# Kernel optimization log

Hardware: AMD Instinct MI355X
Metric: run time of the kernel (lower is better)

The kernel has to match this reference:

```python
import jax, jax.numpy as jnp
import numpy as np

N = 50000          # nodes
E = 800000         # directed edges (before self loops)
H = 2              # attention heads
NEG_SLOPE = 0.2    # PyG GATv2 default
EPS = 1e-5         # GraphNorm eps
DIMS = [(3, 64), (64, 64), (64, 64)]


def _gatv2_layer(x, Wl, Wr, att, b, src, dst):
    # x: [N, din]; Wl, Wr: [din, H*C]; att: [H, C]; b: [C]
    n = x.shape[0]
    h, c = att.shape
    xl = (x @ Wl).reshape(n, h, c)   # source-side transform
    xr = (x @ Wr).reshape(n, h, c)   # target-side transform
    # edge-wise GATv2 score: a . leaky_relu(xl[j] + xr[i])
    e = jax.nn.leaky_relu(xl[src] + xr[dst], NEG_SLOPE)      # [E, H, C]
    logit = jnp.einsum('ehc,hc->eh', e, att)                 # [E, H]
    # segment softmax over incoming edges of each target node
    m = jax.ops.segment_max(logit, dst, num_segments=n)      # [N, H]
    a = jnp.exp(logit - m[dst])
    z = jax.ops.segment_sum(a, dst, num_segments=n)
    alpha = a / z[dst]                                       # [E, H]
    out = jax.ops.segment_sum(alpha[:, :, None] * xl[src], dst, num_segments=n)  # [N, H, C]
    return out.mean(axis=1) + b                              # concat=False -> head mean


def _graph_norm(x, w, b, ms):
    # single-graph GraphNorm: x -> w * (x - ms*mean) / sqrt(var + eps) + b
    mu = x.mean(axis=0)
    o = x - ms * mu
    var = (o * o).mean(axis=0)
    return w * o * jax.lax.rsqrt(var + EPS) + b


def setup_inputs() -> dict:
    key = jax.random.key(0)
    ks = jax.random.split(key, 2 + 3 * len(DIMS))
    inp = {
        'x': jax.random.normal(ks[0], (N, 3), dtype=jnp.float32),
        'edge_index': jax.random.randint(ks[1], (2, E), 0, N, dtype=jnp.int32),
    }
    for i, (din, dout) in enumerate(DIMS, start=1):
        k0, k1, k2 = ks[2 + 3 * (i - 1):2 + 3 * i]
        s_in = np.float32(1.0 / np.sqrt(din))
        s_att = np.float32(1.0 / np.sqrt(dout))
        inp[f'Wl{i}'] = jax.random.normal(k0, (din, H * dout), dtype=jnp.float32) * s_in
        inp[f'Wr{i}'] = jax.random.normal(k1, (din, H * dout), dtype=jnp.float32) * s_in
        inp[f'att{i}'] = jax.random.normal(k2, (H, dout), dtype=jnp.float32) * s_att
        inp[f'b{i}'] = jnp.zeros((dout,), dtype=jnp.float32)
        inp[f'gw{i}'] = jnp.ones((dout,), dtype=jnp.float32)
        inp[f'gb{i}'] = jnp.zeros((dout,), dtype=jnp.float32)
        inp[f'gm{i}'] = jnp.ones((dout,), dtype=jnp.float32)
    return inp


def reference(x, edge_index,
              Wl1, Wr1, att1, b1, gw1, gb1, gm1,
              Wl2, Wr2, att2, b2, gw2, gb2, gm2,
              Wl3, Wr3, att3, b3, gw3, gb3, gm3):
    n = x.shape[0]
    loop = jnp.arange(n, dtype=edge_index.dtype)
    src = jnp.concatenate([edge_index[0], loop])  # add_self_loops=True
    dst = jnp.concatenate([edge_index[1], loop])
    layers = [(Wl1, Wr1, att1, b1, gw1, gb1, gm1),
              (Wl2, Wr2, att2, b2, gw2, gb2, gm2),
              (Wl3, Wr3, att3, b3, gw3, gb3, gm3)]
    for Wl, Wr, att, b, gw, gb, gm in layers:
        x = _gatv2_layer(x, Wl, Wr, att, b, src, dst)
        x = jax.nn.relu(_graph_norm(x, gw, gb, gm))
    return x
```

## Files before the change

kernel.cpp:

```cpp
#include <hip/hip_runtime.h>
#include <math.h>

#define NN 50000
#define NE 800000
#define TE (NE + NN)
#define HC 128
#define NEG_SLOPE 0.2f
#define EPSV 1e-5f
#define NBUCK 64
#define GGRID 782
#define WTB 128
#define ZB 52
#define ZERO_N4 18644

typedef __attribute__((ext_vector_type(8))) short bf16x8;
typedef __attribute__((ext_vector_type(4))) float f32x4;
union BfU { uint4 u; bf16x8 b; };

__device__ __forceinline__ unsigned short f2bf(float x) {
    unsigned u = __float_as_uint(x);
    unsigned r = (u + 0x7fff + ((u >> 16) & 1)) >> 16;
    return (unsigned short)r;
}


__global__ __launch_bounds__(256) void count_k(const int* __restrict__ dst,
                                               int* __restrict__ cnt,
                                               int* __restrict__ rank) {
    int e = blockIdx.x * 256 + threadIdx.x;
    if (e >= TE) return;
    int d = (e < NE) ? dst[e] : (e - NE);
    rank[e] = atomicAdd(&cnt[d], 1);
}

__global__ __launch_bounds__(1024) void scan1_k(const int* __restrict__ cnt,
                                                int* __restrict__ excl,
                                                int* __restrict__ aux) {
    __shared__ int wsum[16];
    int tid = threadIdx.x;
    int gid = blockIdx.x * 1024 + tid;
    int lane = tid & 63, wid = tid >> 6;
    int v = (gid < NN) ? cnt[gid] : 0;
    int x = v;
#pragma unroll
    for (int off = 1; off < 64; off <<= 1) {
        int t = __shfl_up(x, off, 64);
        if (lane >= off) x += t;
    }
    if (lane == 63) wsum[wid] = x;
    __syncthreads();
    if (wid == 0 && lane < 16) {
        int y = wsum[lane];
#pragma unroll
        for (int off = 1; off < 16; off <<= 1) {
            int t = __shfl_up(y, off, 64);
            if (lane >= off) y += t;
        }
        wsum[lane] = y;
    }
    __syncthreads();
    int base = (wid > 0) ? wsum[wid - 1] : 0;
    int incl = base + x;
    if (gid < NN) excl[gid] = incl - v;
    if (tid == 1023) aux[blockIdx.x] = incl;
}

__global__ __launch_bounds__(256) void scatter_k(const int* __restrict__ srcp,
                                                 const int* __restrict__ dstp,
                                                 const int* __restrict__ excl,
                                                 const int* __restrict__ aux,
                                                 const int* __restrict__ rank,
                                                 int* __restrict__ row_ptr,
                                                 int* __restrict__ col,
                                                 int nblk) {
    __shared__ int auxs[64];
    if (threadIdx.x < 64) {
        int lane = threadIdx.x;
        int v = (lane < nblk) ? aux[lane] : 0;
        int x = v;
#pragma unroll
        for (int off = 1; off < 64; off <<= 1) {
            int t = __shfl_up(x, off, 64);
            if (lane >= off) x += t;
        }
        auxs[lane] = x - v;
    }
    __syncthreads();
    int e = blockIdx.x * 256 + threadIdx.x;
    if (e >= TE) return;
    if (e <= NN) row_ptr[e] = (e == NN) ? TE : excl[e] + auxs[e >> 10];
    int s, d;
    if (e < NE) { s = srcp[e]; d = dstp[e]; } else { s = e - NE; d = s; }
    col[excl[d] + auxs[d >> 10] + rank[e]] = s << 8;
}

__device__ __forceinline__ void store_xlp(char* xlp, int row, int c0, const float* a) {
    unsigned hsel = (unsigned)c0 >> 6;
    unsigned dd = (unsigned)c0 & 31;
    unsigned sub = (c0 & 32) ? 2u : 0u;
    char* q = xlp + (size_t)row * 256 + hsel * 128 + 4 * dd + sub;
#pragma unroll
    for (int j = 0; j < 4; ++j)
        *(unsigned short*)(q + 4 * j) = f2bf(a[j]);
}


__global__ __launch_bounds__(256) void init_k(const float* __restrict__ x,
                                              const float* __restrict__ Wl1,
                                              const float* __restrict__ Wr1,
                                              char* __restrict__ xlp,
                                              float* __restrict__ xr,
                                              const float* __restrict__ Wl2,
                                              const float* __restrict__ Wr2,
                                              const float* __restrict__ Wl3,
                                              const float* __restrict__ Wr3,
                                              unsigned short* __restrict__ wt2,
                                              unsigned short* __restrict__ wt3,
                                              float4* __restrict__ zero4) {
    __shared__ float xs[32][72];
    __shared__ float ws[32][260];
    int b = blockIdx.x;
    int tid = threadIdx.x;

    if (b >= GGRID) {
        if (b < GGRID + WTB) {
            int idx = (b - GGRID) * 256 + tid;
            int l = idx >> 14;
            int rem = idx & 16383;
            int k = rem >> 8;
            int c = rem & 255;
            const float* W = (l == 0) ? (c < 128 ? Wl2 : Wr2) : (c < 128 ? Wl3 : Wr3);
            float v = W[k * 128 + (c & 127)];
            unsigned short* wt = (l == 0) ? wt2 : wt3;
            wt[c * 64 + k] = f2bf(v);
        } else {
            float4 zv; zv.x = zv.y = zv.z = zv.w = 0.f;
            for (int i = (b - GGRID - WTB) * 256 + tid; i < ZERO_N4; i += ZB * 256)
                zero4[i] = zv;
        }
        return;
    }

    int row0 = b * 64;
    int row_t = (tid >> 5) * 8;
    int c0 = (tid & 31) * 4;
    const int K = 3;

    float acc0[8][4];
    float acc1[8][4];
#pragma unroll
    for (int i = 0; i < 8; ++i)
#pragma unroll
        for (int j = 0; j < 4; ++j) { acc0[i][j] = 0.f; acc1[i][j] = 0.f; }

    for (int i = tid; i < 64 * K; i += 256) {
        int r = i / K;
        int k = i - r * K;
        int row = row0 + r;
        xs[k][r] = (row < NN) ? x[(size_t)row * K + k] : 0.f;
    }
    for (int i = tid; i < K * 64; i += 256) {
        int k = i >> 6;
        int cq = i & 63;
        const float* srcp = (cq < 32) ? &Wl1[(size_t)k * 128 + cq * 4]
                                      : &Wr1[(size_t)k * 128 + (cq - 32) * 4];
        float4 v = *(const float4*)srcp;
        *(float4*)&ws[k][cq * 4] = v;
    }
    __syncthreads();
    for (int k = 0; k < K; ++k) {
        float4 a0 = *(float4*)&xs[k][row_t];
        float4 a1 = *(float4*)&xs[k][row_t + 4];
        float4 b0 = *(float4*)&ws[k][c0];
        float4 b1 = *(float4*)&ws[k][c0 + 128];
        float av[8] = {a0.x, a0.y, a0.z, a0.w, a1.x, a1.y, a1.z, a1.w};
        float bl[4] = {b0.x, b0.y, b0.z, b0.w};
        float br[4] = {b1.x, b1.y, b1.z, b1.w};
#pragma unroll
        for (int i = 0; i < 8; ++i)
#pragma unroll
            for (int j = 0; j < 4; ++j) {
                acc0[i][j] += av[i] * bl[j];
                acc1[i][j] += av[i] * br[j];
            }
    }
#pragma unroll
    for (int i = 0; i < 8; ++i) {
        int row = row0 + row_t + i;
        if (row < NN) {
            store_xlp(xlp, row, c0, acc0[i]);
            float4 o1; o1.x = acc1[i][0]; o1.y = acc1[i][1]; o1.z = acc1[i][2]; o1.w = acc1[i][3];
            *(float4*)&xr[(size_t)row * HC + c0] = o1;
        }
    }
}

__device__ __forceinline__ void reduce_stats(const float* __restrict__ stats,
                                             const float* __restrict__ gw,
                                             const float* __restrict__ gb,
                                             const float* __restrict__ gm,
                                             float (*part)[128],
                                             float* __restrict__ cf_out) {
    int tid = threadIdx.x;
    int w = tid >> 6;
    int lane = tid & 63;
    float s = 0.f, s2 = 0.f;
    for (int b = 16 * w; b < 16 * w + 16; ++b) {
        s += stats[b * 128 + lane];
        s2 += stats[b * 128 + 64 + lane];
    }
    part[w][lane] = s;
    part[w][64 + lane] = s2;
    __syncthreads();
    if (tid < 64) {
        int c = tid;
        float sum = (part[0][c] + part[1][c]) + (part[2][c] + part[3][c]);
        float sum2 = (part[0][64 + c] + part[1][64 + c]) + (part[2][64 + c] + part[3][64 + c]);
        float inv_n = 1.f / (float)NN;
        float mu = sum * inv_n;
        float ex2 = sum2 * inv_n;
        float g = gm[c];
        float var = ex2 - 2.f * g * mu * mu + g * g * mu * mu;
        float rs = rsqrtf(var + EPSV);
        cf_out[c] = gw[c] * rs;
        cf_out[64 + c] = gb[c] - gw[c] * rs * g * mu;
    }
    __syncthreads();
}


__global__ __launch_bounds__(256) void gemm_mfma(const unsigned* __restrict__ hbf,
                                                 const float* __restrict__ stats,
                                                 const float* __restrict__ gw,
                                                 const float* __restrict__ gb,
                                                 const float* __restrict__ gm,
                                                 const unsigned short* __restrict__ wt,
                                                 char* __restrict__ xlp,
                                                 float* __restrict__ xr,
                                                 int n) {
    __shared__ unsigned short xs[64][72];
    __shared__ float part[4][128];
    __shared__ float cfS[128];
    int tid = threadIdx.x;
    int row0 = blockIdx.x * 64;

    reduce_stats(stats, gw, gb, gm, part, cfS);

    {
        int r = tid >> 2;
        int q = tid & 3;
        int row = row0 + r;
        unsigned pk[8];
        if (row < n) {
            const unsigned* hp = hbf + (size_t)row * 32 + (q & 1) * 16;
            uint4 u0 = *(const uint4*)(hp + 0);
            uint4 u1 = *(const uint4*)(hp + 4);
            uint4 u2 = *(const uint4*)(hp + 8);
            uint4 u3 = *(const uint4*)(hp + 12);
            unsigned hv[16] = {u0.x, u0.y, u0.z, u0.w, u1.x, u1.y, u1.z, u1.w,
                               u2.x, u2.y, u2.z, u2.w, u3.x, u3.y, u3.z, u3.w};
            bool hi = (q >> 1) != 0;
#pragma unroll
            for (int i = 0; i < 4; ++i) {
                float4 v;
                v.x = hi ? __uint_as_float(hv[4 * i + 0] & 0xffff0000u) : __uint_as_float(hv[4 * i + 0] << 16);
                v.y = hi ? __uint_as_float(hv[4 * i + 1] & 0xffff0000u) : __uint_as_float(hv[4 * i + 1] << 16);
                v.z = hi ? __uint_as_float(hv[4 * i + 2] & 0xffff0000u) : __uint_as_float(hv[4 * i + 2] << 16);
                v.w = hi ? __uint_as_float(hv[4 * i + 3] & 0xffff0000u) : __uint_as_float(hv[4 * i + 3] << 16);
                float4 cw = *(const float4*)&cfS[q * 16 + 4 * i];
                float4 cb = *(const float4*)&cfS[64 + q * 16 + 4 * i];
                float r0 = fmaxf(fmaf(cw.x, v.x, cb.x), 0.f);
                float r1 = fmaxf(fmaf(cw.y, v.y, cb.y), 0.f);
                float r2 = fmaxf(fmaf(cw.z, v.z, cb.z), 0.f);
                float r3 = fmaxf(fmaf(cw.w, v.w, cb.w), 0.f);
                pk[2 * i]     = (unsigned)f2bf(r0) | ((unsigned)f2bf(r1) << 16);
                pk[2 * i + 1] = (unsigned)f2bf(r2) | ((unsigned)f2bf(r3) << 16);
            }
        } else {
#pragma unroll
            for (int i = 0; i < 8; ++i) pk[i] = 0;
        }
        uint4* dst = (uint4*)&xs[r][q * 16];
        dst[0] = make_uint4(pk[0], pk[1], pk[2], pk[3]);
        dst[1] = make_uint4(pk[4], pk[5], pk[6], pk[7]);
    }
    __syncthreads();

    int w = tid >> 6;
    int lane = tid & 63;
    int m = lane & 15;
    int quad = lane >> 4;

    BfU a0, a1;
    a0.u = *(const uint4*)&xs[16 * w + m][quad * 8];
    a1.u = *(const uint4*)&xs[16 * w + m][32 + quad * 8];

    const char* wtb = (const char*)wt + (size_t)(m * 128 + quad * 16);

    f32x4 acc[16];
#pragma unroll
    for (int c = 0; c < 16; ++c) acc[c] = (f32x4){0.f, 0.f, 0.f, 0.f};
#pragma unroll
    for (int c = 0; c < 16; ++c) {
        BfU b0, b1;
        b0.u = *(const uint4*)(wtb + c * 2048);
        b1.u = *(const uint4*)(wtb + c * 2048 + 64);
        acc[c] = __builtin_amdgcn_mfma_f32_16x16x32_bf16(a0.b, b0.b, acc[c], 0, 0, 0);
        acc[c] = __builtin_amdgcn_mfma_f32_16x16x32_bf16(a1.b, b1.b, acc[c], 0, 0, 0);
    }

    int rbase = row0 + 16 * w + quad * 4;
#pragma unroll
    for (int c = 8; c < 16; ++c) {
        int colx = 16 * (c - 8) + m;
#pragma unroll
        for (int r = 0; r < 4; ++r) {
            int row = rbase + r;
            if (row < n) xr[(size_t)row * 128 + colx] = acc[c][r];
        }
    }
#pragma unroll
    for (int pi = 0; pi < 4; ++pi) {
        int c = (pi & 1) + (pi >> 1) * 4;
        int head = pi >> 1;
        int dd = (pi & 1) * 16 + m;
#pragma unroll
        for (int r = 0; r < 4; ++r) {
            int row = rbase + r;
            if (row < n) {
                unsigned val = (unsigned)f2bf(acc[c][r]) | ((unsigned)f2bf(acc[c + 2][r]) << 16);
                *(unsigned*)(xlp + (size_t)row * 256 + head * 128 + 4 * dd) = val;
            }
        }
    }
}


__device__ __forceinline__ void unpack8(uint4 q, float* l) {
    l[0] = __uint_as_float(q.x << 16);
    l[1] = __uint_as_float(q.x & 0xffff0000u);
    l[2] = __uint_as_float(q.y << 16);
    l[3] = __uint_as_float(q.y & 0xffff0000u);
    l[4] = __uint_as_float(q.z << 16);
    l[5] = __uint_as_float(q.z & 0xffff0000u);
    l[6] = __uint_as_float(q.w << 16);
    l[7] = __uint_as_float(q.w & 0xffff0000u);
}

__device__ __forceinline__ float logit_part(const float* l,
                                            float4 xv0, float4 xv1,
                                            float4 a0, float4 a1) {
    float u1 = 0.f, u2 = 0.f, t;
    t = l[0] + xv0.x; u1 = fmaf(a0.x, t, u1); u2 = fmaf(a0.x, fabsf(t), u2);
    t = l[1] + xv1.x; u1 = fmaf(a1.x, t, u1); u2 = fmaf(a1.x, fabsf(t), u2);
    t = l[2] + xv0.y; u1 = fmaf(a0.y, t, u1); u2 = fmaf(a0.y, fabsf(t), u2);
    t = l[3] + xv1.y; u1 = fmaf(a1.y, t, u1); u2 = fmaf(a1.y, fabsf(t), u2);
    t = l[4] + xv0.z; u1 = fmaf(a0.z, t, u1); u2 = fmaf(a0.z, fabsf(t), u2);
    t = l[5] + xv1.z; u1 = fmaf(a1.z, t, u1); u2 = fmaf(a1.z, fabsf(t), u2);
    t = l[6] + xv0.w; u1 = fmaf(a0.w, t, u1); u2 = fmaf(a0.w, fabsf(t), u2);
    t = l[7] + xv1.w; u1 = fmaf(a1.w, t, u1); u2 = fmaf(a1.w, fabsf(t), u2);
    return fmaf(0.6f, u1, 0.4f * u2);
}

__device__ __forceinline__ float head_reduce(float x) {
    x += __int_as_float(__builtin_amdgcn_mov_dpp(__float_as_int(x), 0xB1, 0xF, 0xF, true));
    x += __int_as_float(__builtin_amdgcn_mov_dpp(__float_as_int(x), 0x4E, 0xF, 0xF, true));
    x += __shfl_xor(x, 4, 64);
    return x;
}

__device__ __forceinline__ void attn_pair(const char* __restrict__ xlp, int lp16,
                                          int off0, int off1, bool v0, bool v1,
                                          float4 xv0, float4 xv1,
                                          float4 a0, float4 a1,
                                          float* o, float& zacc) {
    uint4 q0 = *(const uint4*)(xlp + (unsigned)(off0 + lp16));
    uint4 q1 = *(const uint4*)(xlp + (unsigned)(off1 + lp16));
    float l0[8], l1[8];
    unpack8(q0, l0);
    unpack8(q1, l1);
    float w0 = head_reduce(logit_part(l0, xv0, xv1, a0, a1));
    float w1 = head_reduce(logit_part(l1, xv0, xv1, a0, a1));
    float e0 = __expf(w0);
    float e1 = __expf(w1);
    if (!v0) e0 = 0.f;
    if (!v1) e1 = 0.f;
    zacc += e0 + e1;
#pragma unroll
    for (int k = 0; k < 8; ++k) o[k] = fmaf(e1, l1[k], fmaf(e0, l0[k], o[k]));
}

__global__ __launch_bounds__(256) void attn_k(const char* __restrict__ xlp,
                                              const float* __restrict__ xr,
                                              const float* __restrict__ att,
                                              const float* __restrict__ bias,
                                              const int* __restrict__ row_ptr,
                                              const int* __restrict__ coloff,
                                              unsigned* __restrict__ hout,
                                              float* __restrict__ stats) {
    __shared__ float sb[4][64];
    int tid = threadIdx.x;
    int lane = tid & 63;
    int wv = tid >> 6;
    int node = blockIdx.x * 4 + wv;
    int t16 = lane & 15;
    int slot = (lane >> 4) * 2;
    int head = t16 >> 3;
    int dd = (t16 & 7) * 4;
    int lp16 = t16 * 16;
    int cbase = head * 64 + dd;

    const float* xrow = xr + (size_t)node * 128;
    float4 xv0 = *(const float4*)(xrow + cbase);
    float4 xv1 = *(const float4*)(xrow + cbase + 32);
    float4 a0 = *(const float4*)(att + cbase);
    float4 a1 = *(const float4*)(att + cbase + 32);

    float o[8];
#pragma unroll
    for (int k = 0; k < 8; ++k) o[k] = 0.f;
    float zacc = 0.f;

    int beg = __builtin_amdgcn_readfirstlane(row_ptr[node]);
    int end = __builtin_amdgcn_readfirstlane(row_ptr[node + 1]);

    int idx = beg;
    for (; idx + 8 <= end; idx += 8) {
        int off0 = coloff[idx + slot];
        int off1 = coloff[idx + slot + 1];
        attn_pair(xlp, lp16, off0, off1, true, true, xv0, xv1, a0, a1, o, zacc);
    }
    if (idx < end) {
        int e1 = end - 1;
        int i0 = idx + slot, i1 = idx + slot + 1;
        int off0 = coloff[min(i0, e1)];
        int off1 = coloff[min(i1, e1)];
        attn_pair(xlp, lp16, off0, off1, i0 < end, i1 < end, xv0, xv1, a0, a1, o, zacc);
    }

    float z = zacc + __shfl_xor(zacc, 16, 64);
    z += __shfl_xor(z, 32, 64);
    float zi = 1.0f / z;
    float r[8];
#pragma unroll
    for (int k = 0; k < 8; ++k) {
        float v = o[k] + __shfl_xor(o[k], 16, 64);
        v += __shfl_xor(v, 32, 64);
        v *= zi;
        float p = __shfl_xor(v, 8, 64);
        r[k] = 0.5f * (v + p);
    }
    if (lane < 8) {
        float4 b0 = *(const float4*)(bias + dd);
        float4 b1 = *(const float4*)(bias + dd + 32);
        float rl0 = r[0] + b0.x, rl1 = r[2] + b0.y, rl2 = r[4] + b0.z, rl3 = r[6] + b0.w;
        float rh0 = r[1] + b1.x, rh1 = r[3] + b1.y, rh2 = r[5] + b1.z, rh3 = r[7] + b1.w;
        unsigned pk0 = (unsigned)f2bf(rl0) | ((unsigned)f2bf(rh0) << 16);
        unsigned pk1 = (unsigned)f2bf(rl1) | ((unsigned)f2bf(rh1) << 16);
        unsigned pk2 = (unsigned)f2bf(rl2) | ((unsigned)f2bf(rh2) << 16);
        unsigned pk3 = (unsigned)f2bf(rl3) | ((unsigned)f2bf(rh3) << 16);
        *(uint4*)&hout[(size_t)node * 32 + dd] = make_uint4(pk0, pk1, pk2, pk3);
        *(float4*)&sb[wv][dd] = make_float4(rl0, rl1, rl2, rl3);
        *(float4*)&sb[wv][dd + 32] = make_float4(rh0, rh1, rh2, rh3);
    }
    __syncthreads();
    if (tid < 64) {
        int c = tid;
        float v0 = sb[0][c], v1 = sb[1][c], v2 = sb[2][c], v3 = sb[3][c];
        float s = (v0 + v1) + (v2 + v3);
        float s2 = fmaf(v0, v0, v1 * v1) + fmaf(v2, v2, v3 * v3);
        float* bkt = stats + (size_t)(blockIdx.x & (NBUCK - 1)) * 128;
        atomicAdd(&bkt[c], s);
        atomicAdd(&bkt[64 + c], s2);
    }
}


__global__ __launch_bounds__(256) void apply_k(const unsigned* __restrict__ h,
                                               const float* __restrict__ stats,
                                               const float* __restrict__ gw,
                                               const float* __restrict__ gb,
                                               const float* __restrict__ gm,
                                               float* __restrict__ y) {
    __shared__ float part[4][128];
    __shared__ float cfS[128];
    reduce_stats(stats, gw, gb, gm, part, cfS);

    int i = blockIdx.x * 256 + threadIdx.x;
    if (i >= NN * 8) return;
    int node = i >> 3;
    int j = (i & 7) * 4;
    uint4 u = *(const uint4*)(h + (size_t)node * 32 + j);
    float4 lo, hi;
    lo.x = __uint_as_float(u.x << 16); hi.x = __uint_as_float(u.x & 0xffff0000u);
    lo.y = __uint_as_float(u.y << 16); hi.y = __uint_as_float(u.y & 0xffff0000u);
    lo.z = __uint_as_float(u.z << 16); hi.z = __uint_as_float(u.z & 0xffff0000u);
    lo.w = __uint_as_float(u.w << 16); hi.w = __uint_as_float(u.w & 0xffff0000u);
    float4 cwl = *(const float4*)&cfS[j];
    float4 cbl = *(const float4*)&cfS[64 + j];
    float4 cwh = *(const float4*)&cfS[32 + j];
    float4 cbh = *(const float4*)&cfS[96 + j];
    float4 rl, rh;
    rl.x = fmaxf(fmaf(cwl.x, lo.x, cbl.x), 0.f);
    rl.y = fmaxf(fmaf(cwl.y, lo.y, cbl.y), 0.f);
    rl.z = fmaxf(fmaf(cwl.z, lo.z, cbl.z), 0.f);
    rl.w = fmaxf(fmaf(cwl.w, lo.w, cbl.w), 0.f);
    rh.x = fmaxf(fmaf(cwh.x, hi.x, cbh.x), 0.f);
    rh.y = fmaxf(fmaf(cwh.y, hi.y, cbh.y), 0.f);
    rh.z = fmaxf(fmaf(cwh.z, hi.z, cbh.z), 0.f);
    rh.w = fmaxf(fmaf(cwh.w, hi.w, cbh.w), 0.f);
    *(float4*)&y[(size_t)node * 64 + j] = rl;
    *(float4*)&y[(size_t)node * 64 + 32 + j] = rh;
}


extern "C" void kernel_launch(void* const* d_in, const int* in_sizes, int n_in,
                              void* d_out, int out_size, void* d_ws, size_t ws_size,
                              hipStream_t stream) {
    const float* x0 = (const float*)d_in[0];
    const int* ei = (const int*)d_in[1];
    const int* srcp = ei;
    const int* dstp = ei + NE;

    const float* Wl[3], *Wr[3], *att[3], *bv[3], *gw[3], *gb[3], *gm[3];
    for (int l = 0; l < 3; ++l) {
        int base = 2 + 7 * l;
        Wl[l] = (const float*)d_in[base + 0];
        Wr[l] = (const float*)d_in[base + 1];
        att[l] = (const float*)d_in[base + 2];
        bv[l] = (const float*)d_in[base + 3];
        gw[l] = (const float*)d_in[base + 4];
        gb[l] = (const float*)d_in[base + 5];
        gm[l] = (const float*)d_in[base + 6];
    }

    char* p = (char*)d_ws;
    auto take = [&](size_t bytes) -> void* {
        void* r = (void*)p;
        p += (bytes + 255) & ~(size_t)255;
        return r;
    };
    char* xlp = (char*)take((size_t)NN * 256);
    float* xr = (float*)take((size_t)NN * 128 * 4);
    unsigned* hb = (unsigned*)take((size_t)NN * 32 * 4);
    char* zr = (char*)take(298304);
    float* stats = (float*)zr;
    int* cnt = (int*)(zr + 98304);
    int* excl = (int*)take((size_t)NN * 4);
    int* row_ptr = (int*)take((size_t)(NN + 1) * 4);
    int* rank = (int*)take((size_t)TE * 4);
    int* col = (int*)take((size_t)TE * 4);
    int* aux = (int*)take(64 * 4);
    unsigned short* wt2 = (unsigned short*)take(16384 * 2);
    unsigned short* wt3 = (unsigned short*)take(16384 * 2);

    int nblk = (NN + 1023) / 1024;
    int egrid = (TE + 255) / 256;

    init_k<<<GGRID + WTB + ZB, 256, 0, stream>>>(x0, Wl[0], Wr[0], xlp, xr,
                                                 Wl[1], Wr[1], Wl[2], Wr[2],
                                                 wt2, wt3, (float4*)zr);
    count_k<<<egrid, 256, 0, stream>>>(dstp, cnt, rank);
    scan1_k<<<nblk, 1024, 0, stream>>>(cnt, excl, aux);
    scatter_k<<<egrid, 256, 0, stream>>>(srcp, dstp, excl, aux, rank, row_ptr, col, nblk);

    int ggrid = (NN + 63) / 64;
    int agrid = NN / 4;
    for (int l = 0; l < 3; ++l) {
        if (l > 0)
            gemm_mfma<<<ggrid, 256, 0, stream>>>(hb, stats + (size_t)(l - 1) * NBUCK * 128,
                                                 gw[l - 1], gb[l - 1], gm[l - 1],
                                                 (l == 1) ? wt2 : wt3, xlp, xr, NN);
        attn_k<<<agrid, 256, 0, stream>>>(xlp, xr, att[l], bv[l], row_ptr, col, hb,
                                          stats + (size_t)l * NBUCK * 128);
    }
    apply_k<<<(NN * 8 + 255) / 256, 256, 0, stream>>>(hb, stats + (size_t)2 * NBUCK * 128,
                                                      gw[2], gb[2], gm[2], (float*)d_out);
}
```

Baseline: 343.0 us.

## Fold leaky-relu and log2e constants into attention weights, hoist final norm coefficients

Pre-scales the attention vector by 0.6*log2e and 0.4*log2e so the per-edge logit drops its final scaling and can use exp2f instead of expf. Sets a launch-bounds occupancy hint of 8 on the attention kernel. Moves the final GraphNorm statistics reduction out of every apply_k block into a single-block coef_k kernel, so each apply block only reads precomputed coefficients, at the cost of one extra launch. No softmax max subtraction is present, so overflow risk is unchanged.

```diff
diff --git a/kernel.cpp b/kernel.cpp
--- a/kernel.cpp
+++ b/kernel.cpp
@@ -336,6 +336,18 @@
 }
 
 
+__global__ __launch_bounds__(256) void coef_k(const float* __restrict__ stats,
+                                              const float* __restrict__ gw,
+                                              const float* __restrict__ gb,
+                                              const float* __restrict__ gm,
+                                              float* __restrict__ cf) {
+    __shared__ float part[4][128];
+    reduce_stats(stats, gw, gb, gm, part, cf);
+}
+
+
+#define L2E 1.4426950408889634f
+
 __device__ __forceinline__ void unpack8(uint4 q, float* l) {
     l[0] = __uint_as_float(q.x << 16);
     l[1] = __uint_as_float(q.x & 0xffff0000u);
@@ -349,17 +361,18 @@
 
 __device__ __forceinline__ float logit_part(const float* l,
                                             float4 xv0, float4 xv1,
-                                            float4 a0, float4 a1) {
+                                            float4 s0, float4 s1,
+                                            float4 q0, float4 q1) {
     float u1 = 0.f, u2 = 0.f, t;
-    t = l[0] + xv0.x; u1 = fmaf(a0.x, t, u1); u2 = fmaf(a0.x, fabsf(t), u2);
-    t = l[1] + xv1.x; u1 = fmaf(a1.x, t, u1); u2 = fmaf(a1.x, fabsf(t), u2);
-    t = l[2] + xv0.y; u1 = fmaf(a0.y, t, u1); u2 = fmaf(a0.y, fabsf(t), u2);
-    t = l[3] + xv1.y; u1 = fmaf(a1.y, t, u1); u2 = fmaf(a1.y, fabsf(t), u2);
-    t = l[4] + xv0.z; u1 = fmaf(a0.z, t, u1); u2 = fmaf(a0.z, fabsf(t), u2);
-    t = l[5] + xv1.z; u1 = fmaf(a1.z, t, u1); u2 = fmaf(a1.z, fabsf(t), u2);
-    t = l[6] + xv0.w; u1 = fmaf(a0.w, t, u1); u2 = fmaf(a0.w, fabsf(t), u2);
-    t = l[7] + xv1.w; u1 = fmaf(a1.w, t, u1); u2 = fmaf(a1.w, fabsf(t), u2);
-    return fmaf(0.6f, u1, 0.4f * u2);
+    t = l[0] + xv0.x; u1 = fmaf(s0.x, t, u1); u2 = fmaf(q0.x, fabsf(t), u2);
+    t = l[1] + xv1.x; u1 = fmaf(s1.x, t, u1); u2 = fmaf(q1.x, fabsf(t), u2);
+    t = l[2] + xv0.y; u1 = fmaf(s0.y, t, u1); u2 = fmaf(q0.y, fabsf(t), u2);
+    t = l[3] + xv1.y; u1 = fmaf(s1.y, t, u1); u2 = fmaf(q1.y, fabsf(t), u2);
+    t = l[4] + xv0.z; u1 = fmaf(s0.z, t, u1); u2 = fmaf(q0.z, fabsf(t), u2);
+    t = l[5] + xv1.z; u1 = fmaf(s1.z, t, u1); u2 = fmaf(q1.z, fabsf(t), u2);
+    t = l[6] + xv0.w; u1 = fmaf(s0.w, t, u1); u2 = fmaf(q0.w, fabsf(t), u2);
+    t = l[7] + xv1.w; u1 = fmaf(s1.w, t, u1); u2 = fmaf(q1.w, fabsf(t), u2);
+    return u1 + u2;
 }
 
 __device__ __forceinline__ float head_reduce(float x) {
@@ -372,17 +385,18 @@
 __device__ __forceinline__ void attn_pair(const char* __restrict__ xlp, int lp16,
                                           int off0, int off1, bool v0, bool v1,
                                           float4 xv0, float4 xv1,
-                                          float4 a0, float4 a1,
+                                          float4 s0, float4 s1,
+                                          float4 q0v, float4 q1v,
                                           float* o, float& zacc) {
-    uint4 q0 = *(const uint4*)(xlp + (unsigned)(off0 + lp16));
-    uint4 q1 = *(const uint4*)(xlp + (unsigned)(off1 + lp16));
+    uint4 g0 = *(const uint4*)(xlp + (unsigned)(off0 + lp16));
+    uint4 g1 = *(const uint4*)(xlp + (unsigned)(off1 + lp16));
     float l0[8], l1[8];
-    unpack8(q0, l0);
-    unpack8(q1, l1);
-    float w0 = head_reduce(logit_part(l0, xv0, xv1, a0, a1));
-    float w1 = head_reduce(logit_part(l1, xv0, xv1, a0, a1));
-    float e0 = __expf(w0);
-    float e1 = __expf(w1);
+    unpack8(g0, l0);
+    unpack8(g1, l1);
+    float w0 = head_reduce(logit_part(l0, xv0, xv1, s0, s1, q0v, q1v));
+    float w1 = head_reduce(logit_part(l1, xv0, xv1, s0, s1, q0v, q1v));
+    float e0 = exp2f(w0);
+    float e1 = exp2f(w1);
     if (!v0) e0 = 0.f;
     if (!v1) e1 = 0.f;
     zacc += e0 + e1;
@@ -390,14 +404,14 @@
     for (int k = 0; k < 8; ++k) o[k] = fmaf(e1, l1[k], fmaf(e0, l0[k], o[k]));
 }
 
-__global__ __launch_bounds__(256) void attn_k(const char* __restrict__ xlp,
-                                              const float* __restrict__ xr,
-                                              const float* __restrict__ att,
-                                              const float* __restrict__ bias,
-                                              const int* __restrict__ row_ptr,
-                                              const int* __restrict__ coloff,
-                                              unsigned* __restrict__ hout,
-                                              float* __restrict__ stats) {
+__global__ __launch_bounds__(256, 8) void attn_k(const char* __restrict__ xlp,
+                                                 const float* __restrict__ xr,
+                                                 const float* __restrict__ att,
+                                                 const float* __restrict__ bias,
+                                                 const int* __restrict__ row_ptr,
+                                                 const int* __restrict__ coloff,
+                                                 unsigned* __restrict__ hout,
+                                                 float* __restrict__ stats) {
     __shared__ float sb[4][64];
     int tid = threadIdx.x;
     int lane = tid & 63;
@@ -415,6 +429,12 @@
     float4 xv1 = *(const float4*)(xrow + cbase + 32);
     float4 a0 = *(const float4*)(att + cbase);
     float4 a1 = *(const float4*)(att + cbase + 32);
+    const float c6 = 0.6f * L2E, c4 = 0.4f * L2E;
+    float4 s0, s1, q0v, q1v;
+    s0.x = c6 * a0.x; s0.y = c6 * a0.y; s0.z = c6 * a0.z; s0.w = c6 * a0.w;
+    s1.x = c6 * a1.x; s1.y = c6 * a1.y; s1.z = c6 * a1.z; s1.w = c6 * a1.w;
+    q0v.x = c4 * a0.x; q0v.y = c4 * a0.y; q0v.z = c4 * a0.z; q0v.w = c4 * a0.w;
+    q1v.x = c4 * a1.x; q1v.y = c4 * a1.y; q1v.z = c4 * a1.z; q1v.w = c4 * a1.w;
 
     float o[8];
 #pragma unroll
@@ -428,14 +448,14 @@
     for (; idx + 8 <= end; idx += 8) {
         int off0 = coloff[idx + slot];
         int off1 = coloff[idx + slot + 1];
-        attn_pair(xlp, lp16, off0, off1, true, true, xv0, xv1, a0, a1, o, zacc);
+        attn_pair(xlp, lp16, off0, off1, true, true, xv0, xv1, s0, s1, q0v, q1v, o, zacc);
     }
     if (idx < end) {
         int e1 = end - 1;
         int i0 = idx + slot, i1 = idx + slot + 1;
         int off0 = coloff[min(i0, e1)];
         int off1 = coloff[min(i1, e1)];
-        attn_pair(xlp, lp16, off0, off1, i0 < end, i1 < end, xv0, xv1, a0, a1, o, zacc);
+        attn_pair(xlp, lp16, off0, off1, i0 < end, i1 < end, xv0, xv1, s0, s1, q0v, q1v, o, zacc);
     }
 
     float z = zacc + __shfl_xor(zacc, 16, 64);
@@ -477,15 +497,8 @@
 
 
 __global__ __launch_bounds__(256) void apply_k(const unsigned* __restrict__ h,
-                                               const float* __restrict__ stats,
-                                               const float* __restrict__ gw,
-                                               const float* __restrict__ gb,
-                                               const float* __restrict__ gm,
+                                               const float* __restrict__ cf,
                                                float* __restrict__ y) {
-    __shared__ float part[4][128];
-    __shared__ float cfS[128];
-    reduce_stats(stats, gw, gb, gm, part, cfS);
-
     int i = blockIdx.x * 256 + threadIdx.x;
     if (i >= NN * 8) return;
     int node = i >> 3;
@@ -496,10 +509,10 @@
     lo.y = __uint_as_float(u.y << 16); hi.y = __uint_as_float(u.y & 0xffff0000u);
     lo.z = __uint_as_float(u.z << 16); hi.z = __uint_as_float(u.z & 0xffff0000u);
     lo.w = __uint_as_float(u.w << 16); hi.w = __uint_as_float(u.w & 0xffff0000u);
-    float4 cwl = *(const float4*)&cfS[j];
-    float4 cbl = *(const float4*)&cfS[64 + j];
-    float4 cwh = *(const float4*)&cfS[32 + j];
-    float4 cbh = *(const float4*)&cfS[96 + j];
+    float4 cwl = *(const float4*)&cf[j];
+    float4 cbl = *(const float4*)&cf[64 + j];
+    float4 cwh = *(const float4*)&cf[32 + j];
+    float4 cbh = *(const float4*)&cf[96 + j];
     float4 rl, rh;
     rl.x = fmaxf(fmaf(cwl.x, lo.x, cbl.x), 0.f);
     rl.y = fmaxf(fmaf(cwl.y, lo.y, cbl.y), 0.f);
@@ -551,6 +564,7 @@
     int* rank = (int*)take((size_t)TE * 4);
     int* col = (int*)take((size_t)TE * 4);
     int* aux = (int*)take(64 * 4);
+    float* cf3 = (float*)take(128 * 4);
     unsigned short* wt2 = (unsigned short*)take(16384 * 2);
     unsigned short* wt3 = (unsigned short*)take(16384 * 2);
 
@@ -574,6 +588,6 @@
         attn_k<<<agrid, 256, 0, stream>>>(xlp, xr, att[l], bv[l], row_ptr, col, hb,
                                           stats + (size_t)l * NBUCK * 128);
     }
-    apply_k<<<(NN * 8 + 255) / 256, 256, 0, stream>>>(hb, stats + (size_t)2 * NBUCK * 128,
-                                                      gw[2], gb[2], gm[2], (float*)d_out);
-}
+    coef_k<<<1, 256, 0, stream>>>(stats + (size_t)2 * NBUCK * 128, gw[2], gb[2], gm[2], cf3);
+    apply_k<<<(NN * 8 + 255) / 256, 256, 0, stream>>>(hb, cf3, (float*)d_out);
+}
```

Result: slower. 357.4 us (+4.2%).
